# Optimization experiments

Measured on AMD Instinct MI355X. Metric: run time of the kernel, lower is better.

The kernel has to match this reference:

```python
import jax, jax.numpy as jnp
import numpy as np

N_NODES = 50000


def gcn_norm(edge_index, edge_weight, n):
    """PyG GCNConv normalization: add self-loops (weight 1), sym-normalize."""
    src, dst = edge_index[0], edge_index[1]
    loop = jnp.arange(n, dtype=src.dtype)
    src = jnp.concatenate([src, loop])
    dst = jnp.concatenate([dst, loop])
    w = jnp.concatenate([edge_weight, jnp.ones((n,), dtype=edge_weight.dtype)])
    deg = jax.ops.segment_sum(w, dst, num_segments=n)  # in-degree w/ self-loops
    dis = jnp.where(deg > 0, jax.lax.rsqrt(deg), 0.0)  # deg^{-1/2}, inf -> 0
    norm = dis[src] * w * dis[dst]                      # [E+N]
    return src, dst, norm


def gcn_conv(x, src, dst, norm, W, b):
    h = x @ W                                            # [N, F_out]
    msg = norm[:, None] * h[src]                         # gather + scale
    out = jax.ops.segment_sum(msg, dst, num_segments=x.shape[0])  # scatter-add
    return out + b


def setup_inputs() -> dict:
    key = jax.random.key(0)
    ks = jax.random.split(key, 10)
    n, e = N_NODES, 800000
    in_dim, hidden, out_dim = 256, 128, 64
    x = jax.random.normal(ks[0], (n, in_dim), dtype=jnp.float32)
    edge_index = jax.random.randint(ks[1], (2, e), 0, n, dtype=jnp.int32)
    edge_weight = jax.random.uniform(ks[2], (e,), dtype=jnp.float32)
    def glorot(k, fi, fo):
        lim = float(np.sqrt(6.0 / (fi + fo)))
        return jax.random.uniform(k, (fi, fo), minval=-lim, maxval=lim, dtype=jnp.float32)
    return {
        "x": x, "edge_index": edge_index, "edge_weight": edge_weight,
        "W1": glorot(ks[3], in_dim, hidden), "b1": jnp.zeros((hidden,), jnp.float32),
        "W2": glorot(ks[4], hidden, hidden), "b2": jnp.zeros((hidden,), jnp.float32),
        "W3": glorot(ks[5], hidden, out_dim), "b3": jnp.zeros((out_dim,), jnp.float32),
    }


def reference(x, edge_index, edge_weight, W1, b1, W2, b2, W3, b3):
    n = x.shape[0]
    src, dst, norm = gcn_norm(edge_index, edge_weight, n)  # cached=True: shared
    h = jax.nn.relu(gcn_conv(x, src, dst, norm, W1, b1))   # dropout: eval mode no-op
    h = jax.nn.relu(gcn_conv(h, src, dst, norm, W2, b2))
    h = gcn_conv(h, src, dst, norm, W3, b3)
    return h
```

## Files before the change

kernel.cpp:

```cpp
#include <hip/hip_runtime.h>
#include <hip/hip_bf16.h>
#include <stdint.h>

#define NODES 50000
#define EDGES 800000
#define R_REP 8
#define SCAN_TB 256
#define SCAN_NB ((NODES + SCAN_TB - 1) / SCAN_TB)

typedef short bf16x8 __attribute__((ext_vector_type(8)));
typedef float f32x4 __attribute__((ext_vector_type(4)));

__device__ __forceinline__ unsigned short f2bf(float f) {
    union { float f; unsigned u; } v; v.f = f;
    unsigned r = v.u + 0x7fff + ((v.u >> 16) & 1);
    return (unsigned short)(r >> 16);
}
__device__ __forceinline__ float bf2f(unsigned short h) {
    union { float f; unsigned u; } v; v.u = ((unsigned)h) << 16;
    return v.f;
}
__device__ __forceinline__ float bflo(unsigned hv) {
    union { float f; unsigned u; } v; v.u = hv << 16;
    return v.f;
}
__device__ __forceinline__ float bfhi(unsigned hv) {
    union { float f; unsigned u; } v; v.u = hv & 0xffff0000u;
    return v.f;
}


__device__ __forceinline__ void wfrag_one(const float* __restrict__ W, unsigned short* Wf,
                                          int idx, int K, int Nn) {
    int NT = Nn >> 4;
    int lane = idx & 63;
    int f = idx >> 6;
    int nt = f % NT;
    int k0 = (f / NT) << 5;
    int n = (nt << 4) + (lane & 15);
    int kk = k0 + ((lane >> 4) << 3);
    unsigned short o[8];
#pragma unroll
    for (int j = 0; j < 8; j++) o[j] = f2bf(W[(kk + j) * Nn + n]);
    ((uint4*)Wf)[idx] = *(uint4*)o;
}

__global__ void k_setup(unsigned long long* packed,
                        const float* __restrict__ W1, unsigned short* Wf1,
                        const float* __restrict__ W2, unsigned short* Wf2,
                        const float* __restrict__ W3, unsigned short* Wf3) {
    int idx = blockIdx.x * blockDim.x + threadIdx.x;
    if (idx < NODES * R_REP) { packed[idx] = 0ull; return; }
    int k = idx - NODES * R_REP;
    if (k < 4096) wfrag_one(W1, Wf1, k, 256, 128);
    else if (k < 6144) wfrag_one(W2, Wf2, k - 4096, 128, 128);
    else if (k < 7168) wfrag_one(W3, Wf3, k - 6144, 128, 64);
}

__global__ void k_deg(const int* __restrict__ dst, const float* __restrict__ w,
                      unsigned long long* __restrict__ packed, int* __restrict__ rank) {
    int e = blockIdx.x * blockDim.x + threadIdx.x;
    int r = blockIdx.x & (R_REP - 1);
    if (e < EDGES) {
        int d = dst[e];
        unsigned fx = __float2uint_rn(w[e] * 16777216.0f);
        unsigned long long add = (1ull << 40) | (unsigned long long)fx;
        unsigned long long old = atomicAdd(&packed[(size_t)r * NODES + d], add);
        rank[e] = (int)(old >> 40);
    }
}


__global__ void k_scan1(const unsigned long long* __restrict__ packed,
                        float* __restrict__ dis, int* __restrict__ repoff,
                        int* __restrict__ pre, int* __restrict__ bsum) {
    __shared__ int sm[SCAN_TB];
    int t = threadIdx.x;
    int i = blockIdx.x * SCAN_TB + t;
    int v = 0;
    if (i < NODES) {
        unsigned long long degfx = 0;
        int off = 0;
#pragma unroll
        for (int r = 0; r < R_REP; r++) {
            unsigned long long pk = packed[(size_t)r * NODES + i];
            repoff[(size_t)r * NODES + i] = off;
            off += (int)(pk >> 40);
            degfx += (pk & 0xFFFFFFFFFFull);
        }
        v = off;
        float deg = 1.0f + (float)degfx * (1.0f / 16777216.0f);
        dis[i] = rsqrtf(deg);
    }
    sm[t] = v;
    __syncthreads();
    for (int off = 1; off < SCAN_TB; off <<= 1) {
        int x = (t >= off) ? sm[t - off] : 0;
        __syncthreads();
        sm[t] += x;
        __syncthreads();
    }
    if (i < NODES) pre[i] = sm[t] - v;
    if (t == SCAN_TB - 1) bsum[blockIdx.x] = sm[t];
}

__global__ void k_scan2(const int* __restrict__ bsum, int* __restrict__ boff,
                        int* __restrict__ rowptr) {
    __shared__ int sm[256];
    int t = threadIdx.x;
    int v = (t < SCAN_NB) ? bsum[t] : 0;
    sm[t] = v;
    __syncthreads();
    for (int off = 1; off < 256; off <<= 1) {
        int x = (t >= off) ? sm[t - off] : 0;
        __syncthreads();
        sm[t] += x;
        __syncthreads();
    }
    if (t < SCAN_NB) boff[t] = sm[t] - v;
    if (t == 255) rowptr[NODES] = sm[255];
}

__global__ void k_scatter(const int* __restrict__ src, const int* __restrict__ dst,
                          const float* __restrict__ w, const float* __restrict__ dis,
                          const int* __restrict__ pre, const int* __restrict__ boff,
                          const int* __restrict__ repoff, const int* __restrict__ rank,
                          int2* __restrict__ rec, int* __restrict__ rowptr) {
    int e = blockIdx.x * blockDim.x + threadIdx.x;
    int r = blockIdx.x & (R_REP - 1);
    if (e < NODES) rowptr[e] = pre[e] + boff[e >> 8];
    if (e < EDGES) {
        int s = src[e], d = dst[e];
        float nrm = dis[s] * w[e] * dis[d];
        int pos = pre[d] + boff[d >> 8] + repoff[(size_t)r * NODES + d] + rank[e];
        int2 rc; rc.x = s; rc.y = __float_as_int(nrm);
        rec[pos] = rc;
    }
}

template <int K, int Nn, bool A_F32>
__global__ void k_gemm(const void* __restrict__ A_, const uint4* __restrict__ Wf,
                       unsigned short* __restrict__ Hout) {
    constexpr int NT = Nn / 16;
    int lane = threadIdx.x & 63;
    int wave = threadIdx.x >> 6;
    int tile = blockIdx.x * 4 + wave;
    if (tile * 16 >= NODES) return;
    int row = tile * 16 + (lane & 15);
    int kbase = (lane >> 4) * 8;

    f32x4 acc[NT];
#pragma unroll
    for (int i = 0; i < NT; i++) acc[i] = (f32x4){0.f, 0.f, 0.f, 0.f};

    for (int k0 = 0; k0 < K; k0 += 32) {
        bf16x8 a;
        if (A_F32) {
            const float* A = (const float*)A_;
            const float4* p = (const float4*)&A[(size_t)row * K + k0 + kbase];
            float4 u0 = p[0], u1 = p[1];
            unsigned short t[8];
            t[0] = f2bf(u0.x); t[1] = f2bf(u0.y); t[2] = f2bf(u0.z); t[3] = f2bf(u0.w);
            t[4] = f2bf(u1.x); t[5] = f2bf(u1.y); t[6] = f2bf(u1.z); t[7] = f2bf(u1.w);
            a = *(bf16x8*)t;
        } else {
            const unsigned short* A = (const unsigned short*)A_;
            a = *(const bf16x8*)&A[(size_t)row * K + k0 + kbase];
        }
        int fbase = (k0 >> 5) * NT;
#pragma unroll
        for (int nt = 0; nt < NT; nt++) {
            uint4 braw = Wf[(fbase + nt) * 64 + lane];
            bf16x8 b = *(bf16x8*)&braw;
            acc[nt] = __builtin_amdgcn_mfma_f32_16x16x32_bf16(a, b, acc[nt], 0, 0, 0);
        }
    }
    int r0 = (lane >> 4) * 4;
    int col = lane & 15;
#pragma unroll
    for (int nt = 0; nt < NT; nt++) {
#pragma unroll
        for (int r = 0; r < 4; r++) {
            int m = tile * 16 + r0 + r;
            Hout[(size_t)m * Nn + nt * 16 + col] = f2bf(acc[nt][r]);
        }
    }
}

template <int F, bool RELU, bool OUT_F32>
__global__ void k_agg(const unsigned short* __restrict__ H, const int2* __restrict__ rec,
                      const int* __restrict__ rowptr, const float* __restrict__ dis,
                      const float* __restrict__ bias, void* __restrict__ out_) {
    constexpr int VPT = F / 64;
    int lane = threadIdx.x & 63;
    int node = blockIdx.x * 4 + (threadIdx.x >> 6);
    if (node >= NODES) return;
    node = __builtin_amdgcn_readfirstlane(node);

    const unsigned* H32 = (const unsigned*)H;

    float sn = dis[node]; sn = sn * sn;
    float acc0, acc1 = 0.f;
    if (VPT == 2) {
        unsigned hv = H32[node * 64 + lane];
        acc0 = sn * bflo(hv);
        acc1 = sn * bfhi(hv);
    } else {
        acc0 = sn * bf2f(H[node * 64 + lane]);
    }

    int beg = rowptr[node], end = rowptr[node + 1];
    for (int j = beg; j < end; j += 8) {
        int ss[8]; float nn[8];
#pragma unroll
        for (int q = 0; q < 8; q++) {
            int idx = j + q;
            idx = (idx < end - 1) ? idx : (end - 1);
            int2 rc = rec[idx];
            ss[q] = rc.x;
            nn[q] = (j + q < end) ? __int_as_float(rc.y) : 0.0f;
        }
        if (VPT == 2) {
            unsigned hh[8];
#pragma unroll
            for (int q = 0; q < 8; q++) hh[q] = H32[ss[q] * 64 + lane];
#pragma unroll
            for (int q = 0; q < 8; q++) {
                acc0 += nn[q] * bflo(hh[q]);
                acc1 += nn[q] * bfhi(hh[q]);
            }
        } else {
            unsigned short hh[8];
#pragma unroll
            for (int q = 0; q < 8; q++) hh[q] = H[ss[q] * 64 + lane];
#pragma unroll
            for (int q = 0; q < 8; q++) acc0 += nn[q] * bf2f(hh[q]);
        }
    }

    if (OUT_F32) {
        float* out = (float*)out_;
        if (VPT == 2) {
            float x0 = acc0 + bias[lane * 2];
            float x1 = acc1 + bias[lane * 2 + 1];
            if (RELU) { x0 = fmaxf(x0, 0.f); x1 = fmaxf(x1, 0.f); }
            out[(size_t)node * F + lane * 2] = x0;
            out[(size_t)node * F + lane * 2 + 1] = x1;
        } else {
            float x0 = acc0 + bias[lane];
            if (RELU) x0 = fmaxf(x0, 0.f);
            out[(size_t)node * F + lane] = x0;
        }
    } else {
        unsigned short* out = (unsigned short*)out_;
        if (VPT == 2) {
            float x0 = acc0 + bias[lane * 2];
            float x1 = acc1 + bias[lane * 2 + 1];
            if (RELU) { x0 = fmaxf(x0, 0.f); x1 = fmaxf(x1, 0.f); }
            unsigned packed = (unsigned)f2bf(x0) | ((unsigned)f2bf(x1) << 16);
            *(unsigned*)&out[(size_t)node * F + lane * 2] = packed;
        } else {
            float x0 = acc0 + bias[lane];
            if (RELU) x0 = fmaxf(x0, 0.f);
            out[(size_t)node * F + lane] = f2bf(x0);
        }
    }
}


extern "C" void kernel_launch(void* const* d_in, const int* in_sizes, int n_in,
                              void* d_out, int out_size, void* d_ws, size_t ws_size,
                              hipStream_t stream) {
    const float* x  = (const float*)d_in[0];
    const int*   ei = (const int*)d_in[1];
    const float* w  = (const float*)d_in[2];
    const float* W1 = (const float*)d_in[3];
    const float* b1 = (const float*)d_in[4];
    const float* W2 = (const float*)d_in[5];
    const float* b2 = (const float*)d_in[6];
    const float* W3 = (const float*)d_in[7];
    const float* b3 = (const float*)d_in[8];
    const int* src = ei;
    const int* dst = ei + EDGES;

    char* p = (char*)d_ws;
    auto alloc = [&](size_t n) { char* r = p; p += (n + 511) & ~(size_t)511; return r; };
    unsigned long long* packed = (unsigned long long*)alloc((size_t)NODES * R_REP * 8);
    float*          dis    = (float*)alloc(NODES * 4);
    int*            rowptr = (int*)alloc((NODES + 1) * 4);
    int*            repoff = (int*)alloc((size_t)NODES * R_REP * 4);
    int*            rank   = (int*)alloc(EDGES * 4);
    int*            pre    = (int*)alloc(NODES * 4);
    int*            bsum   = (int*)alloc(SCAN_NB * 4);
    int*            boff   = (int*)alloc(SCAN_NB * 4);
    int2*           rec    = (int2*)alloc(EDGES * 8);
    unsigned short* h      = (unsigned short*)alloc((size_t)NODES * 128 * 2);
    unsigned short* xb     = (unsigned short*)alloc((size_t)NODES * 128 * 2);
    unsigned short* wf1    = (unsigned short*)alloc(256 * 128 * 2);
    unsigned short* wf2    = (unsigned short*)alloc(128 * 128 * 2);
    unsigned short* wf3    = (unsigned short*)alloc(128 * 64 * 2);

    const int TB = 256;
    int nb_setup = (NODES * R_REP + 7168 + TB - 1) / TB;
    int nb_edges = (EDGES + TB - 1) / TB;

    hipLaunchKernelGGL(k_setup, dim3(nb_setup), dim3(TB), 0, stream, packed, W1, wf1, W2, wf2, W3, wf3);
    hipLaunchKernelGGL(k_deg, dim3(nb_edges), dim3(TB), 0, stream, dst, w, packed, rank);
    hipLaunchKernelGGL(k_scan1, dim3(SCAN_NB), dim3(SCAN_TB), 0, stream, packed, dis, repoff, pre, bsum);
    hipLaunchKernelGGL(k_scan2, dim3(1), dim3(256), 0, stream, bsum, boff, rowptr);
    hipLaunchKernelGGL(k_scatter, dim3(nb_edges), dim3(TB), 0, stream, src, dst, w, dis,
                       pre, boff, repoff, rank, rec, rowptr);

    int nb_gemm = (NODES / 16 + 3) / 4;
    int nb_agg  = (NODES + 3) / 4;

    hipLaunchKernelGGL((k_gemm<256, 128, true>), dim3(nb_gemm), dim3(TB), 0, stream, (const void*)x, (const uint4*)wf1, h);
    hipLaunchKernelGGL((k_agg<128, true, false>), dim3(nb_agg), dim3(TB), 0, stream, h, rec, rowptr, dis, b1, (void*)xb);

    hipLaunchKernelGGL((k_gemm<128, 128, false>), dim3(nb_gemm), dim3(TB), 0, stream, (const void*)xb, (const uint4*)wf2, h);
    hipLaunchKernelGGL((k_agg<128, true, false>), dim3(nb_agg), dim3(TB), 0, stream, h, rec, rowptr, dis, b2, (void*)xb);

    hipLaunchKernelGGL((k_gemm<128, 64, false>), dim3(nb_gemm), dim3(TB), 0, stream, (const void*)xb, (const uint4*)wf3, h);
    hipLaunchKernelGGL((k_agg<64, false, true>), dim3(nb_agg), dim3(TB), 0, stream, h, rec, rowptr, dis, b3, d_out);
}
```

Before: 290.3 us.

## Prefetch next edge batch in aggregation and interleave degree counters per node

The gather-aggregate loop now processes 16 edges per iteration and loads the next batch's indices and weights before issuing feature gathers for the current batch, a software pipeline meant to hide edge-record load latency. Source indices are made wave-uniform with readfirstlane so address arithmetic can use scalar registers. Separately, the replicated degree counters are laid out node-major ([node][rep]) instead of rep-major, so the scan reads 8 contiguous words per node. The changes add register pressure, which may lower occupancy, and waste gather work on low-degree nodes because of the 16-edge padding.

```diff
diff --git a/kernel.cpp b/kernel.cpp
--- a/kernel.cpp
+++ b/kernel.cpp
@@ -65,7 +65,7 @@
         int d = dst[e];
         unsigned fx = __float2uint_rn(w[e] * 16777216.0f);
         unsigned long long add = (1ull << 40) | (unsigned long long)fx;
-        unsigned long long old = atomicAdd(&packed[(size_t)r * NODES + d], add);
+        unsigned long long old = atomicAdd(&packed[(size_t)d * R_REP + r], add);
         rank[e] = (int)(old >> 40);
     }
 }
@@ -83,7 +83,7 @@
         int off = 0;
 #pragma unroll
         for (int r = 0; r < R_REP; r++) {
-            unsigned long long pk = packed[(size_t)r * NODES + i];
+            unsigned long long pk = packed[(size_t)i * R_REP + r];
             repoff[(size_t)r * NODES + i] = off;
             off += (int)(pk >> 40);
             degfx += (pk & 0xFFFFFFFFFFull);
@@ -210,31 +210,48 @@
     }
 
     int beg = rowptr[node], end = rowptr[node + 1];
-    for (int j = beg; j < end; j += 8) {
-        int ss[8]; float nn[8];
-#pragma unroll
-        for (int q = 0; q < 8; q++) {
-            int idx = j + q;
-            idx = (idx < end - 1) ? idx : (end - 1);
-            int2 rc = rec[idx];
-            ss[q] = rc.x;
-            nn[q] = (j + q < end) ? __int_as_float(rc.y) : 0.0f;
+    int last = end - 1;
+
+    int cs[16]; float cn[16];
+#pragma unroll
+    for (int q = 0; q < 16; q++) {
+        int idx = beg + q; idx = (idx < last) ? idx : last;
+        int2 rc = rec[idx];
+        cs[q] = __builtin_amdgcn_readfirstlane(rc.x);
+        cn[q] = (beg + q < end) ? __int_as_float(rc.y) : 0.0f;
+    }
+
+    for (int j = beg; j < end; j += 16) {
+        int ns[16]; float nn[16];
+        int jn = j + 16;
+        if (jn < end) {
+#pragma unroll
+            for (int q = 0; q < 16; q++) {
+                int idx = jn + q; idx = (idx < last) ? idx : last;
+                int2 rc = rec[idx];
+                ns[q] = __builtin_amdgcn_readfirstlane(rc.x);
+                nn[q] = (jn + q < end) ? __int_as_float(rc.y) : 0.0f;
+            }
         }
         if (VPT == 2) {
-            unsigned hh[8];
-#pragma unroll
-            for (int q = 0; q < 8; q++) hh[q] = H32[ss[q] * 64 + lane];
-#pragma unroll
-            for (int q = 0; q < 8; q++) {
-                acc0 += nn[q] * bflo(hh[q]);
-                acc1 += nn[q] * bfhi(hh[q]);
+            unsigned hh[16];
+#pragma unroll
+            for (int q = 0; q < 16; q++) hh[q] = H32[cs[q] * 64 + lane];
+#pragma unroll
+            for (int q = 0; q < 16; q++) {
+                acc0 += cn[q] * bflo(hh[q]);
+                acc1 += cn[q] * bfhi(hh[q]);
             }
         } else {
-            unsigned short hh[8];
-#pragma unroll
-            for (int q = 0; q < 8; q++) hh[q] = H[ss[q] * 64 + lane];
-#pragma unroll
-            for (int q = 0; q < 8; q++) acc0 += nn[q] * bf2f(hh[q]);
+            unsigned short hh[16];
+#pragma unroll
+            for (int q = 0; q < 16; q++) hh[q] = H[cs[q] * 64 + lane];
+#pragma unroll
+            for (int q = 0; q < 16; q++) acc0 += cn[q] * bf2f(hh[q]);
+        }
+        if (jn < end) {
+#pragma unroll
+            for (int q = 0; q < 16; q++) { cs[q] = ns[q]; cn[q] = nn[q]; }
         }
     }
 
```

After: 303.5 us. 1.05x slower.

## Vectorize aggregation gathers to 16-byte rows and interleave degree replicas

Applied to the files above, without the earlier changes.

The aggregation kernel now has groups of lanes each gather a full neighbor row with 16-byte loads, splitting the edges of a node across several lane groups and combining them with xor-shuffle reductions. One lane group then adds the self-loop term and bias and writes 8 features per lane. Separately, the replicated degree counters move from a replica-major to a node-major layout, so the 8 replicas of a node share a cache line. This aims to cut the number of memory transactions per edge and to improve gather parallelism, at the cost of extra shuffle reductions and idle lanes in the epilogue.

```diff
diff --git a/kernel.cpp b/kernel.cpp
--- a/kernel.cpp
+++ b/kernel.cpp
@@ -28,7 +28,6 @@
     union { float f; unsigned u; } v; v.u = hv & 0xffff0000u;
     return v.f;
 }
-
 
 __device__ __forceinline__ void wfrag_one(const float* __restrict__ W, unsigned short* Wf,
                                           int idx, int K, int Nn) {
@@ -65,11 +64,10 @@
         int d = dst[e];
         unsigned fx = __float2uint_rn(w[e] * 16777216.0f);
         unsigned long long add = (1ull << 40) | (unsigned long long)fx;
-        unsigned long long old = atomicAdd(&packed[(size_t)r * NODES + d], add);
+        unsigned long long old = atomicAdd(&packed[(size_t)d * R_REP + r], add);
         rank[e] = (int)(old >> 40);
     }
 }
-
 
 __global__ void k_scan1(const unsigned long long* __restrict__ packed,
                         float* __restrict__ dis, int* __restrict__ repoff,
@@ -83,7 +81,7 @@
         int off = 0;
 #pragma unroll
         for (int r = 0; r < R_REP; r++) {
-            unsigned long long pk = packed[(size_t)r * NODES + i];
+            unsigned long long pk = packed[(size_t)i * R_REP + r];
             repoff[(size_t)r * NODES + i] = off;
             off += (int)(pk >> 40);
             degfx += (pk & 0xFFFFFFFFFFull);
@@ -191,78 +189,77 @@
 __global__ void k_agg(const unsigned short* __restrict__ H, const int2* __restrict__ rec,
                       const int* __restrict__ rowptr, const float* __restrict__ dis,
                       const float* __restrict__ bias, void* __restrict__ out_) {
-    constexpr int VPT = F / 64;
+    constexpr int LPG = F / 8;
+    constexpr int GRP = 64 / LPG;
     int lane = threadIdx.x & 63;
     int node = blockIdx.x * 4 + (threadIdx.x >> 6);
     if (node >= NODES) return;
     node = __builtin_amdgcn_readfirstlane(node);
 
-    const unsigned* H32 = (const unsigned*)H;
-
-    float sn = dis[node]; sn = sn * sn;
-    float acc0, acc1 = 0.f;
-    if (VPT == 2) {
-        unsigned hv = H32[node * 64 + lane];
-        acc0 = sn * bflo(hv);
-        acc1 = sn * bfhi(hv);
-    } else {
-        acc0 = sn * bf2f(H[node * 64 + lane]);
-    }
+    int g  = lane / LPG;
+    int fl = lane % LPG;
+
+    const uint4* Hq = (const uint4*)H;
+    constexpr int RQ = F / 8;
+
+    float acc[8];
+#pragma unroll
+    for (int k = 0; k < 8; k++) acc[k] = 0.f;
 
     int beg = rowptr[node], end = rowptr[node + 1];
-    for (int j = beg; j < end; j += 8) {
-        int ss[8]; float nn[8];
-#pragma unroll
-        for (int q = 0; q < 8; q++) {
-            int idx = j + q;
-            idx = (idx < end - 1) ? idx : (end - 1);
-            int2 rc = rec[idx];
-            ss[q] = rc.x;
-            nn[q] = (j + q < end) ? __int_as_float(rc.y) : 0.0f;
-        }
-        if (VPT == 2) {
-            unsigned hh[8];
-#pragma unroll
-            for (int q = 0; q < 8; q++) hh[q] = H32[ss[q] * 64 + lane];
-#pragma unroll
-            for (int q = 0; q < 8; q++) {
-                acc0 += nn[q] * bflo(hh[q]);
-                acc1 += nn[q] * bfhi(hh[q]);
-            }
+    int last = end - 1;
+
+    for (int c = beg; c < end; c += 4 * GRP) {
+        uint4 hv[4]; float nm[4];
+#pragma unroll
+        for (int d = 0; d < 4; d++) {
+            int idx = c + d * GRP + g;
+            int cidx = (idx < last) ? idx : last;
+            int2 rc = rec[cidx];
+            nm[d] = (idx < end) ? __int_as_float(rc.y) : 0.0f;
+            hv[d] = Hq[(size_t)rc.x * RQ + fl];
+        }
+#pragma unroll
+        for (int d = 0; d < 4; d++) {
+            acc[0] += nm[d] * bflo(hv[d].x); acc[1] += nm[d] * bfhi(hv[d].x);
+            acc[2] += nm[d] * bflo(hv[d].y); acc[3] += nm[d] * bfhi(hv[d].y);
+            acc[4] += nm[d] * bflo(hv[d].z); acc[5] += nm[d] * bfhi(hv[d].z);
+            acc[6] += nm[d] * bflo(hv[d].w); acc[7] += nm[d] * bfhi(hv[d].w);
+        }
+    }
+
+#pragma unroll
+    for (int off = LPG; off < 64; off <<= 1) {
+#pragma unroll
+        for (int k = 0; k < 8; k++) acc[k] += __shfl_xor(acc[k], off);
+    }
+
+    if (lane < LPG) {
+        float sn = dis[node]; sn = sn * sn;
+        uint4 sv = Hq[(size_t)node * RQ + fl];
+        acc[0] += sn * bflo(sv.x); acc[1] += sn * bfhi(sv.x);
+        acc[2] += sn * bflo(sv.y); acc[3] += sn * bfhi(sv.y);
+        acc[4] += sn * bflo(sv.z); acc[5] += sn * bfhi(sv.z);
+        acc[6] += sn * bflo(sv.w); acc[7] += sn * bfhi(sv.w);
+        float4 bl = ((const float4*)bias)[fl * 2];
+        float4 bh = ((const float4*)bias)[fl * 2 + 1];
+        acc[0] += bl.x; acc[1] += bl.y; acc[2] += bl.z; acc[3] += bl.w;
+        acc[4] += bh.x; acc[5] += bh.y; acc[6] += bh.z; acc[7] += bh.w;
+        if (RELU) {
+#pragma unroll
+            for (int k = 0; k < 8; k++) acc[k] = fmaxf(acc[k], 0.f);
+        }
+        if (OUT_F32) {
+            float4* out = (float4*)out_;
+            float4 o0 = {acc[0], acc[1], acc[2], acc[3]};
+            float4 o1 = {acc[4], acc[5], acc[6], acc[7]};
+            out[(size_t)node * (F / 4) + fl * 2] = o0;
+            out[(size_t)node * (F / 4) + fl * 2 + 1] = o1;
         } else {
-            unsigned short hh[8];
-#pragma unroll
-            for (int q = 0; q < 8; q++) hh[q] = H[ss[q] * 64 + lane];
-#pragma unroll
-            for (int q = 0; q < 8; q++) acc0 += nn[q] * bf2f(hh[q]);
-        }
-    }
-
-    if (OUT_F32) {
-        float* out = (float*)out_;
-        if (VPT == 2) {
-            float x0 = acc0 + bias[lane * 2];
-            float x1 = acc1 + bias[lane * 2 + 1];
-            if (RELU) { x0 = fmaxf(x0, 0.f); x1 = fmaxf(x1, 0.f); }
-            out[(size_t)node * F + lane * 2] = x0;
-            out[(size_t)node * F + lane * 2 + 1] = x1;
-        } else {
-            float x0 = acc0 + bias[lane];
-            if (RELU) x0 = fmaxf(x0, 0.f);
-            out[(size_t)node * F + lane] = x0;
-        }
-    } else {
-        unsigned short* out = (unsigned short*)out_;
-        if (VPT == 2) {
-            float x0 = acc0 + bias[lane * 2];
-            float x1 = acc1 + bias[lane * 2 + 1];
-            if (RELU) { x0 = fmaxf(x0, 0.f); x1 = fmaxf(x1, 0.f); }
-            unsigned packed = (unsigned)f2bf(x0) | ((unsigned)f2bf(x1) << 16);
-            *(unsigned*)&out[(size_t)node * F + lane * 2] = packed;
-        } else {
-            float x0 = acc0 + bias[lane];
-            if (RELU) x0 = fmaxf(x0, 0.f);
-            out[(size_t)node * F + lane] = f2bf(x0);
+            unsigned short o[8];
+#pragma unroll
+            for (int k = 0; k < 8; k++) o[k] = f2bf(acc[k]);
+            ((uint4*)out_)[(size_t)node * RQ + fl] = *(uint4*)o;
         }
     }
 }
```

Result: slower. 300.6 us (+3.6%).
